# Optimization experiments

Measured on AMD Instinct MI355X. Metric: run time of the kernel, lower is better.

Reference implementation:

```python
import jax, jax.numpy as jnp
import numpy as np

EMBED_DIM = 512
U_EMBED = 6
NUM_HEADS = 8
HEAD_DIM = EMBED_DIM // NUM_HEADS
SCALE = HEAD_DIM ** -0.5
BS, N = 8, 1024


def setup_inputs() -> dict:
    key = jax.random.key(0)
    ks = jax.random.split(key, 9)
    x = jax.random.normal(ks[0], (BS, N, EMBED_DIM), dtype=jnp.float32)
    u = jax.random.normal(ks[1], (BS, U_EMBED, N, N), dtype=jnp.float32)
    umask = jax.random.randint(ks[2], (BS, N, N, 1), 0, 2).astype(bool)
    s = EMBED_DIM ** -0.5
    Wq = jax.random.normal(ks[3], (EMBED_DIM, EMBED_DIM), dtype=jnp.float32) * s
    Wk = jax.random.normal(ks[4], (EMBED_DIM, EMBED_DIM), dtype=jnp.float32) * s
    Wv = jax.random.normal(ks[5], (EMBED_DIM, EMBED_DIM), dtype=jnp.float32) * s
    Wu = jax.random.normal(ks[6], (NUM_HEADS, U_EMBED), dtype=jnp.float32) * (U_EMBED ** -0.5)
    bu = jnp.zeros((NUM_HEADS,), dtype=jnp.float32)
    Wo = jax.random.normal(ks[7], (EMBED_DIM, EMBED_DIM), dtype=jnp.float32) * s
    bo = jnp.zeros((EMBED_DIM,), dtype=jnp.float32)
    return {"x": x, "u": u, "umask": umask, "Wq": Wq, "Wk": Wk, "Wv": Wv,
            "Wu": Wu, "bu": bu, "Wo": Wo, "bo": bo}


def reference(x, u, umask, Wq, Wk, Wv, Wu, bu, Wo, bo):
    bs, n, _ = x.shape
    # projections (torch Linear: y = x @ W.T)
    Q = (x @ Wq.T).reshape(bs, n, NUM_HEADS, HEAD_DIM)
    K = (x @ Wk.T).reshape(bs, n, NUM_HEADS, HEAD_DIM)
    V = (x @ Wv.T).reshape(bs, n, NUM_HEADS, HEAD_DIM)
    # scores: [bs, H, N, N]
    scores = jnp.einsum('bqhd,bkhd->bhqk', Q, K) * SCALE
    # 1x1 conv bias: [bs, u_embed, N, N] -> [bs, H, N, N]
    ub = jnp.einsum('bunm,hu->bhnm', u, Wu) + bu[None, :, None, None]
    # umask: [bs, N, N, 1] -> transpose(3,1) -> [bs, 1, N, N]
    m = jnp.transpose(umask, (0, 3, 2, 1))
    ub = jnp.where(m, -jnp.inf, ub)
    scores = scores + ub
    attn = jax.nn.softmax(scores, axis=-1)
    ctx = jnp.einsum('bhqk,bkhd->bqhd', attn, V).reshape(bs, n, EMBED_DIM)
    out = ctx @ Wo.T + bo
    return out, attn
```

## Files before the change

### kernel.cpp

```cpp
#include <hip/hip_runtime.h>
#include <hip/hip_bf16.h>
#include <math.h>

#define BSZ 8
#define SEQ 1024
#define EMB 512
#define NH 8
#define HD 64
#define UE 6
#define QKSCALE 0.125f

typedef unsigned short u16;
typedef short bf16x8 __attribute__((ext_vector_type(8)));
typedef float f32x4 __attribute__((ext_vector_type(4)));
typedef unsigned short ushort4_t __attribute__((ext_vector_type(4)));

__device__ __forceinline__ u16 f2bf(float f) {
  unsigned u = __float_as_uint(f);
  unsigned r = (u + 0x7fffu + ((u >> 16) & 1u)) >> 16;
  return (u16)r;
}
__device__ __forceinline__ void f2hl(float f, u16& hi, u16& lo) {
  hi = f2bf(f);
  float fh = __uint_as_float(((unsigned)hi) << 16);
  lo = f2bf(f - fh);
}
#define F2HL_V(fv, hv, lv, idx)            \
  {                                        \
    u16 _h, _l;                            \
    f2hl((fv), _h, _l);                    \
    (hv)[idx] = (short)_h;                 \
    (lv)[idx] = (short)_l;                 \
  }
__device__ __forceinline__ f32x4 mfma_bf16(bf16x8 a, bf16x8 b, f32x4 c) {
  return __builtin_amdgcn_mfma_f32_16x16x32_bf16(a, b, c, 0, 0, 0);
}

__global__ __launch_bounds__(256) void split_kernel(const float* __restrict__ src,
                                                    u16* __restrict__ hi, u16* __restrict__ lo, int n4) {
  int i = blockIdx.x * 256 + threadIdx.x;
  if (i >= n4) return;
  float4 v = ((const float4*)src)[i];
  ushort4_t h, l;
  F2HL_V(v.x, h, l, 0); F2HL_V(v.y, h, l, 1);
  F2HL_V(v.z, h, l, 2); F2HL_V(v.w, h, l, 3);
  ((ushort4_t*)hi)[i] = h;
  ((ushort4_t*)lo)[i] = l;
}

__global__ __launch_bounds__(256, 2) void qkv_mfma_kernel(
    const float* __restrict__ x, const u16* __restrict__ Wsp,
    u16* __restrict__ Qhi, u16* __restrict__ Qlo,
    u16* __restrict__ Khi, u16* __restrict__ Klo, u16* __restrict__ Vt) {
  const int mt = blockIdx.x, h = blockIdx.y, wsel = blockIdx.z;
  const int m0 = mt * 64, c0 = h * 64;
  const u16* __restrict__ WH = Wsp + (size_t)wsel * 524288;
  const u16* __restrict__ WL = WH + 262144;
  __shared__ u16 AH[64][40], AL[64][40], BH[64][40], BL[64][40];
  __shared__ u16 vout[64][69];
  const int t = threadIdx.x, w = t >> 6, l = t & 63;
  const int wr = (w >> 1) * 32, wc = (w & 1) * 32;
  f32x4 acc[2][2] = {};
  const int srow = t >> 2;
  for (int e0 = 0; e0 < EMB; e0 += 32) {
    {
      const int c = (t & 3) * 8;
      float4 v0 = *(const float4*)&x[(size_t)(m0 + srow) * EMB + e0 + c];
      float4 v1 = *(const float4*)&x[(size_t)(m0 + srow) * EMB + e0 + c + 4];
      ushort4_t h0, l0, h1, l1;
      F2HL_V(v0.x, h0, l0, 0); F2HL_V(v0.y, h0, l0, 1); F2HL_V(v0.z, h0, l0, 2); F2HL_V(v0.w, h0, l0, 3);
      F2HL_V(v1.x, h1, l1, 0); F2HL_V(v1.y, h1, l1, 1); F2HL_V(v1.z, h1, l1, 2); F2HL_V(v1.w, h1, l1, 3);
      *(ushort4_t*)&AH[srow][c] = h0; *(ushort4_t*)&AH[srow][c + 4] = h1;
      *(ushort4_t*)&AL[srow][c] = l0; *(ushort4_t*)&AL[srow][c + 4] = l1;
      *(bf16x8*)&BH[srow][c] = *(const bf16x8*)&WH[(size_t)(c0 + srow) * EMB + e0 + c];
      *(bf16x8*)&BL[srow][c] = *(const bf16x8*)&WL[(size_t)(c0 + srow) * EMB + e0 + c];
    }
    __syncthreads();
    const int ar = l & 15, ach = (l >> 4) << 3;
    bf16x8 ah0 = *(bf16x8*)&AH[wr + ar][ach],      ah1 = *(bf16x8*)&AH[wr + 16 + ar][ach];
    bf16x8 al0 = *(bf16x8*)&AL[wr + ar][ach],      al1 = *(bf16x8*)&AL[wr + 16 + ar][ach];
    bf16x8 bh0 = *(bf16x8*)&BH[wc + ar][ach],      bh1 = *(bf16x8*)&BH[wc + 16 + ar][ach];
    bf16x8 bl0 = *(bf16x8*)&BL[wc + ar][ach],      bl1 = *(bf16x8*)&BL[wc + 16 + ar][ach];
    acc[0][0] = mfma_bf16(ah0, bh0, acc[0][0]); acc[0][0] = mfma_bf16(ah0, bl0, acc[0][0]); acc[0][0] = mfma_bf16(al0, bh0, acc[0][0]);
    acc[0][1] = mfma_bf16(ah0, bh1, acc[0][1]); acc[0][1] = mfma_bf16(ah0, bl1, acc[0][1]); acc[0][1] = mfma_bf16(al0, bh1, acc[0][1]);
    acc[1][0] = mfma_bf16(ah1, bh0, acc[1][0]); acc[1][0] = mfma_bf16(ah1, bl0, acc[1][0]); acc[1][0] = mfma_bf16(al1, bh0, acc[1][0]);
    acc[1][1] = mfma_bf16(ah1, bh1, acc[1][1]); acc[1][1] = mfma_bf16(ah1, bl1, acc[1][1]); acc[1][1] = mfma_bf16(al1, bh1, acc[1][1]);
    __syncthreads();
  }
  const int bb = m0 >> 10, n0 = m0 & 1023;
  if (wsel < 2) {
    u16* __restrict__ OH = wsel ? Khi : Qhi;
    u16* __restrict__ OL = wsel ? Klo : Qlo;
#pragma unroll
    for (int i = 0; i < 2; ++i)
#pragma unroll
      for (int j = 0; j < 2; ++j) {
        const int col = wc + 16 * j + (l & 15);
#pragma unroll
        for (int r = 0; r < 4; ++r) {
          const int n = n0 + wr + 16 * i + ((l >> 4) << 2) + r;
          size_t o = ((size_t)(bb * NH + h) * SEQ + n) * HD + col;
          u16 hi, lo; f2hl(acc[i][j][r], hi, lo);
          OH[o] = hi; OL[o] = lo;
        }
      }
  } else {
#pragma unroll
    for (int i = 0; i < 2; ++i)
#pragma unroll
      for (int j = 0; j < 2; ++j) {
        const int col = wc + 16 * j + (l & 15);
#pragma unroll
        for (int r = 0; r < 4; ++r)
          vout[wr + 16 * i + ((l >> 4) << 2) + r][col] = f2bf(acc[i][j][r]);
      }
    __syncthreads();
    const int d = t >> 2, nch = (t & 3) * 16;
    bf16x8 o0, o1;
#pragma unroll
    for (int i = 0; i < 8; ++i) o0[i] = (short)vout[nch + i][d];
#pragma unroll
    for (int i = 0; i < 8; ++i) o1[i] = (short)vout[nch + 8 + i][d];
    size_t dst = ((size_t)(bb * NH + h) * HD + d) * SEQ + n0 + nch;
    *(bf16x8*)&Vt[dst] = o0;
    *(bf16x8*)&Vt[dst + 8] = o1;
  }
}

__global__ __launch_bounds__(256, 2) void scores_kernel(
    const u16* __restrict__ Qhi, const u16* __restrict__ Qlo,
    const u16* __restrict__ Khi, const u16* __restrict__ Klo,
    const float* __restrict__ u, const int* __restrict__ umask,
    const float* __restrict__ Wu, const float* __restrict__ bu,
    float* __restrict__ attn, float2* __restrict__ pairs) {
  const int kt = blockIdx.x, qt = blockIdx.y, b = blockIdx.z;
  const int q0 = qt * 64, k0 = kt * 64;
  __shared__ u16 KsH[64][72], KsL[64][72];
  __shared__ unsigned char ms[64][68];
  const int t = threadIdx.x, w = t >> 6, l = t & 63;
  const int qb = 16 * w + ((l >> 4) << 2);
  const int kl = l & 15;

#pragma unroll
  for (int r = 0; r < 16; ++r) {
    int idx = r * 256 + t; int k = idx >> 6, q = idx & 63;
    ms[k][q] = (unsigned char)(umask[((size_t)b * SEQ + k0 + k) * SEQ + q0 + q] != 0);
  }

  unsigned upk[UE][4][2];
  {
    const float* ubase = u + ((size_t)b * UE * SEQ + q0 + qb) * SEQ + k0 + kl;
#pragma unroll
    for (int uu = 0; uu < UE; ++uu)
#pragma unroll
      for (int tt = 0; tt < 4; ++tt)
#pragma unroll
        for (int p = 0; p < 2; ++p) {
          const float* up = ubase + (size_t)uu * SEQ * SEQ + (size_t)(2 * p) * SEQ + 16 * tt;
          float f0 = up[0], f1 = up[SEQ];
          upk[uu][tt][p] = (unsigned)f2bf(f0) | ((unsigned)f2bf(f1) << 16);
        }
  }

  const int krow_s = t >> 2, kc_s = (t & 3) * 16;
  bf16x8 kpre0, kpre1, kpre2, kpre3;
  {
    const u16* kp = Khi + ((size_t)(b * NH) * SEQ + k0 + krow_s) * HD + kc_s;
    const u16* kq = Klo + ((size_t)(b * NH) * SEQ + k0 + krow_s) * HD + kc_s;
    kpre0 = *(const bf16x8*)kp; kpre1 = *(const bf16x8*)(kp + 8);
    kpre2 = *(const bf16x8*)kq; kpre3 = *(const bf16x8*)(kq + 8);
  }

  for (int h = 0; h < NH; ++h) {
    const int bh = b * NH + h;
    __syncthreads();
    *(bf16x8*)&KsH[krow_s][kc_s] = kpre0;
    *(bf16x8*)&KsH[krow_s][kc_s + 8] = kpre1;
    *(bf16x8*)&KsL[krow_s][kc_s] = kpre2;
    *(bf16x8*)&KsL[krow_s][kc_s + 8] = kpre3;
    if (h < NH - 1) {
      const u16* kp = Khi + ((size_t)(bh + 1) * SEQ + k0 + krow_s) * HD + kc_s;
      const u16* kq = Klo + ((size_t)(bh + 1) * SEQ + k0 + krow_s) * HD + kc_s;
      kpre0 = *(const bf16x8*)kp; kpre1 = *(const bf16x8*)(kp + 8);
      kpre2 = *(const bf16x8*)kq; kpre3 = *(const bf16x8*)(kq + 8);
    }
    __syncthreads();

    const u16* qp = Qhi + ((size_t)bh * SEQ + q0 + 16 * w + (l & 15)) * HD + ((l >> 4) << 3);
    const u16* ql = Qlo + ((size_t)bh * SEQ + q0 + 16 * w + (l & 15)) * HD + ((l >> 4) << 3);
    bf16x8 qh0 = *(const bf16x8*)qp, qh1 = *(const bf16x8*)(qp + 32);
    bf16x8 ql0 = *(const bf16x8*)ql, ql1 = *(const bf16x8*)(ql + 32);
    float wu_[UE];
#pragma unroll
    for (int uu = 0; uu < UE; ++uu) wu_[uu] = Wu[h * UE + uu];
    const float bub = bu[h];
    float* abase = attn + ((size_t)bh * SEQ + q0 + qb) * SEQ + k0 + kl;

    float sv[4][4];
#pragma unroll
    for (int tt = 0; tt < 4; ++tt) {
      const int krow = tt * 16 + (l & 15), kch = (l >> 4) << 3;
      bf16x8 kh0 = *(bf16x8*)&KsH[krow][kch], kh1 = *(bf16x8*)&KsH[krow][kch + 32];
      bf16x8 kl0 = *(bf16x8*)&KsL[krow][kch], kl1 = *(bf16x8*)&KsL[krow][kch + 32];
      f32x4 acc = {0.f, 0.f, 0.f, 0.f};
      acc = mfma_bf16(qh0, kh0, acc); acc = mfma_bf16(qh1, kh1, acc);
      acc = mfma_bf16(qh0, kl0, acc); acc = mfma_bf16(qh1, kl1, acc);
      acc = mfma_bf16(ql0, kh0, acc); acc = mfma_bf16(ql1, kh1, acc);
#pragma unroll
      for (int p = 0; p < 2; ++p) {
        float ubx = bub, uby = bub;
#pragma unroll
        for (int uu = 0; uu < UE; ++uu) {
          unsigned pk = upk[uu][tt][p];
          float flo = __uint_as_float(pk << 16);
          float fhi = __uint_as_float(pk & 0xffff0000u);
          ubx = fmaf(wu_[uu], flo, ubx);
          uby = fmaf(wu_[uu], fhi, uby);
        }
        sv[2 * p + 0][tt] = ms[tt * 16 + kl][qb + 2 * p + 0] ? -INFINITY : acc[2 * p + 0] * QKSCALE + ubx;
        sv[2 * p + 1][tt] = ms[tt * 16 + kl][qb + 2 * p + 1] ? -INFINITY : acc[2 * p + 1] * QKSCALE + uby;
      }
    }
#pragma unroll
    for (int r = 0; r < 4; ++r)
#pragma unroll
      for (int tt = 0; tt < 4; ++tt)
        abase[(size_t)r * SEQ + tt * 16] = sv[r][tt];
#pragma unroll
    for (int r = 0; r < 4; ++r) {
      float m = fmaxf(fmaxf(sv[r][0], sv[r][1]), fmaxf(sv[r][2], sv[r][3]));
#pragma unroll
      for (int o = 1; o <= 8; o <<= 1) m = fmaxf(m, __shfl_xor(m, o));
      float s = __expf(sv[r][0] - m) + __expf(sv[r][1] - m) +
                __expf(sv[r][2] - m) + __expf(sv[r][3] - m);
#pragma unroll
      for (int o = 1; o <= 8; o <<= 1) s += __shfl_xor(s, o);
      if (kl == 0)
        pairs[((size_t)bh * SEQ + q0 + qb + r) * 16 + kt] = make_float2(m, s);
    }
  }
}

__global__ __launch_bounds__(256, 2) void pv_softmax_kernel(
    float* __restrict__ attn, const u16* __restrict__ Vt,
    const float2* __restrict__ pairs, u16* __restrict__ ctx) {
  const int qt = blockIdx.x, bh = blockIdx.y;
  const int q0 = qt * 64;
  __shared__ u16 Pl[64][72], Vs[64][72];
  const int t = threadIdx.x, w = t >> 6, l = t & 63;
  const int row = t >> 2, cc = (t & 3) * 16;
  float* arow = attn + ((size_t)bh * SEQ + q0 + row) * SEQ + cc;

  float M = -INFINITY, S = 0.f;
  {
    const float2* pp = pairs + ((size_t)bh * SEQ + q0 + row) * 16 + (t & 3) * 4;
#pragma unroll
    for (int j = 0; j < 4; ++j) {
      float2 c = pp[j];
      float Mn = fmaxf(M, c.x);
      S = S * __expf(M - Mn) + c.y * __expf(c.x - Mn);
      M = Mn;
    }
#pragma unroll
    for (int o = 1; o <= 2; o <<= 1) {
      float Mo = __shfl_xor(M, o), So = __shfl_xor(S, o);
      float Mn = fmaxf(M, Mo);
      S = S * __expf(M - Mn) + So * __expf(Mo - Mn);
      M = Mn;
    }
  }
  const float inv = 1.0f / S;

  const int wr = (w >> 1) * 32, wc = (w & 1) * 32;
  f32x4 acc[2][2] = {};
  float4 va0 = *(const float4*)(arow + 0), va1 = *(const float4*)(arow + 4);
  float4 va2 = *(const float4*)(arow + 8), va3 = *(const float4*)(arow + 12);
  const u16* vrow = Vt + ((size_t)bh * HD + row) * SEQ + cc;
  bf16x8 vb0 = *(const bf16x8*)vrow, vb1 = *(const bf16x8*)(vrow + 8);

  for (int k0 = 0; k0 < SEQ; k0 += 64) {
    bf16x8 p0, p1;
    float4 p;
    p.x = __expf(va0.x - M) * inv; p.y = __expf(va0.y - M) * inv;
    p.z = __expf(va0.z - M) * inv; p.w = __expf(va0.w - M) * inv;
    *(float4*)(arow + k0 + 0) = p;
    p0[0] = (short)f2bf(p.x); p0[1] = (short)f2bf(p.y); p0[2] = (short)f2bf(p.z); p0[3] = (short)f2bf(p.w);
    p.x = __expf(va1.x - M) * inv; p.y = __expf(va1.y - M) * inv;
    p.z = __expf(va1.z - M) * inv; p.w = __expf(va1.w - M) * inv;
    *(float4*)(arow + k0 + 4) = p;
    p0[4] = (short)f2bf(p.x); p0[5] = (short)f2bf(p.y); p0[6] = (short)f2bf(p.z); p0[7] = (short)f2bf(p.w);
    p.x = __expf(va2.x - M) * inv; p.y = __expf(va2.y - M) * inv;
    p.z = __expf(va2.z - M) * inv; p.w = __expf(va2.w - M) * inv;
    *(float4*)(arow + k0 + 8) = p;
    p1[0] = (short)f2bf(p.x); p1[1] = (short)f2bf(p.y); p1[2] = (short)f2bf(p.z); p1[3] = (short)f2bf(p.w);
    p.x = __expf(va3.x - M) * inv; p.y = __expf(va3.y - M) * inv;
    p.z = __expf(va3.z - M) * inv; p.w = __expf(va3.w - M) * inv;
    *(float4*)(arow + k0 + 12) = p;
    p1[4] = (short)f2bf(p.x); p1[5] = (short)f2bf(p.y); p1[6] = (short)f2bf(p.z); p1[7] = (short)f2bf(p.w);

    *(bf16x8*)&Pl[row][cc] = p0;
    *(bf16x8*)&Pl[row][cc + 8] = p1;
    *(bf16x8*)&Vs[row][cc] = vb0;
    *(bf16x8*)&Vs[row][cc + 8] = vb1;

    if (k0 + 64 < SEQ) {
      va0 = *(const float4*)(arow + k0 + 64);
      va1 = *(const float4*)(arow + k0 + 68);
      va2 = *(const float4*)(arow + k0 + 72);
      va3 = *(const float4*)(arow + k0 + 76);
      vb0 = *(const bf16x8*)(vrow + k0 + 64);
      vb1 = *(const bf16x8*)(vrow + k0 + 72);
    }
    __syncthreads();
#pragma unroll
    for (int kb = 0; kb < 2; ++kb) {
      const int kch = kb * 32 + ((l >> 4) << 3);
      bf16x8 a0 = *(bf16x8*)&Pl[wr + (l & 15)][kch];
      bf16x8 a1 = *(bf16x8*)&Pl[wr + 16 + (l & 15)][kch];
      bf16x8 b0 = *(bf16x8*)&Vs[wc + (l & 15)][kch];
      bf16x8 b1 = *(bf16x8*)&Vs[wc + 16 + (l & 15)][kch];
      acc[0][0] = mfma_bf16(a0, b0, acc[0][0]);
      acc[0][1] = mfma_bf16(a0, b1, acc[0][1]);
      acc[1][0] = mfma_bf16(a1, b0, acc[1][0]);
      acc[1][1] = mfma_bf16(a1, b1, acc[1][1]);
    }
    __syncthreads();
  }
  const int b = bh >> 3, h = bh & 7;
#pragma unroll
  for (int i = 0; i < 2; ++i)
#pragma unroll
    for (int j = 0; j < 2; ++j) {
      const int d = h * HD + wc + 16 * j + (l & 15);
#pragma unroll
      for (int r = 0; r < 4; ++r) {
        const int q = q0 + wr + 16 * i + ((l >> 4) << 2) + r;
        ctx[((size_t)(b * SEQ + q)) * EMB + d] = f2bf(acc[i][j][r]);
      }
    }
}

__global__ __launch_bounds__(256, 2) void oproj_kernel(
    const u16* __restrict__ ctx,
    const u16* __restrict__ WoH, const u16* __restrict__ WoL,
    const float* __restrict__ bo, float* __restrict__ out) {
  const int mt = blockIdx.x, ct = blockIdx.y;
  const int m0 = mt * 64, c0 = ct * 64;
  __shared__ u16 AH[64][40], BH[64][40], BL[64][40];
  const int t = threadIdx.x, w = t >> 6, l = t & 63;
  const int wr = (w >> 1) * 32, wc = (w & 1) * 32;
  f32x4 acc[2][2] = {};
  const int srow = t >> 2, sc = (t & 3) * 8;
  for (int e0 = 0; e0 < EMB; e0 += 32) {
    *(bf16x8*)&AH[srow][sc] = *(const bf16x8*)&ctx[(size_t)(m0 + srow) * EMB + e0 + sc];
    *(bf16x8*)&BH[srow][sc] = *(const bf16x8*)&WoH[(size_t)(c0 + srow) * EMB + e0 + sc];
    *(bf16x8*)&BL[srow][sc] = *(const bf16x8*)&WoL[(size_t)(c0 + srow) * EMB + e0 + sc];
    __syncthreads();
    const int ar = l & 15, ach = (l >> 4) << 3;
    bf16x8 ah0 = *(bf16x8*)&AH[wr + ar][ach],      ah1 = *(bf16x8*)&AH[wr + 16 + ar][ach];
    bf16x8 bh0 = *(bf16x8*)&BH[wc + ar][ach],      bh1 = *(bf16x8*)&BH[wc + 16 + ar][ach];
    bf16x8 bl0 = *(bf16x8*)&BL[wc + ar][ach],      bl1 = *(bf16x8*)&BL[wc + 16 + ar][ach];
    acc[0][0] = mfma_bf16(ah0, bh0, acc[0][0]); acc[0][0] = mfma_bf16(ah0, bl0, acc[0][0]);
    acc[0][1] = mfma_bf16(ah0, bh1, acc[0][1]); acc[0][1] = mfma_bf16(ah0, bl1, acc[0][1]);
    acc[1][0] = mfma_bf16(ah1, bh0, acc[1][0]); acc[1][0] = mfma_bf16(ah1, bl0, acc[1][0]);
    acc[1][1] = mfma_bf16(ah1, bh1, acc[1][1]); acc[1][1] = mfma_bf16(ah1, bl1, acc[1][1]);
    __syncthreads();
  }
#pragma unroll
  for (int i = 0; i < 2; ++i)
#pragma unroll
    for (int j = 0; j < 2; ++j) {
      const int col = c0 + wc + 16 * j + (l & 15);
      const float bias = bo[col];
#pragma unroll
      for (int r = 0; r < 4; ++r) {
        const int m = m0 + wr + 16 * i + ((l >> 4) << 2) + r;
        out[(size_t)m * EMB + col] = acc[i][j][r] + bias;
      }
    }
}

extern "C" void kernel_launch(void* const* d_in, const int* in_sizes, int n_in,
                              void* d_out, int out_size, void* d_ws, size_t ws_size,
                              hipStream_t stream) {
  const float* x = (const float*)d_in[0];
  const float* u = (const float*)d_in[1];
  const int* umask = (const int*)d_in[2];
  const float* Wq = (const float*)d_in[3];
  const float* Wk = (const float*)d_in[4];
  const float* Wv = (const float*)d_in[5];
  const float* Wu = (const float*)d_in[6];
  const float* bu = (const float*)d_in[7];
  const float* Wo = (const float*)d_in[8];
  const float* bo = (const float*)d_in[9];

  float* out = (float*)d_out;
  float* attn = out + (size_t)BSZ * SEQ * EMB;

  const size_t per = (size_t)BSZ * NH * SEQ * HD;
  u16* ws = (u16*)d_ws;
  u16* Qhi = ws;
  u16* Qlo = Qhi + per;
  u16* Khi = Qlo + per;
  u16* Klo = Khi + per;
  u16* Vt = Klo + per;
  u16* ctx = Vt + per;
  float2* pairs = (float2*)(ctx + per);
  u16* Wsp = (u16*)((char*)pairs + (size_t)BSZ * NH * SEQ * 16 * sizeof(float2));

  const int wn4 = 262144 / 4;
  split_kernel<<<dim3(wn4 / 256), 256, 0, stream>>>(Wq, Wsp + 0 * 524288, Wsp + 0 * 524288 + 262144, wn4);
  split_kernel<<<dim3(wn4 / 256), 256, 0, stream>>>(Wk, Wsp + 1 * 524288, Wsp + 1 * 524288 + 262144, wn4);
  split_kernel<<<dim3(wn4 / 256), 256, 0, stream>>>(Wv, Wsp + 2 * 524288, Wsp + 2 * 524288 + 262144, wn4);
  split_kernel<<<dim3(wn4 / 256), 256, 0, stream>>>(Wo, Wsp + 3 * 524288, Wsp + 3 * 524288 + 262144, wn4);

  qkv_mfma_kernel<<<dim3(128, 8, 3), 256, 0, stream>>>(x, Wsp, Qhi, Qlo, Khi, Klo, Vt);
  scores_kernel<<<dim3(16, 16, 8), 256, 0, stream>>>(Qhi, Qlo, Khi, Klo, u, umask, Wu, bu, attn, pairs);
  pv_softmax_kernel<<<dim3(16, 64), 256, 0, stream>>>(attn, Vt, pairs, ctx);
  oproj_kernel<<<dim3(128, 8), 256, 0, stream>>>(ctx, Wsp + 3 * 524288, Wsp + 3 * 524288 + 262144, bo, out);
}
```

Before: 421.7 us.

## Store unnormalized bf16 exp scores in-place in attn upper half, drop max tracking

The scores kernel now writes exp(score) directly as bf16 into the upper half of each attn row's float storage and records per-tile plain sums, dropping the running max. The pv kernel reads these bf16 values instead of fp32 scores, writes normalized fp32 attn, and applies 1/sum to the context accumulator at the end. K staging through shared memory is removed in favour of direct global loads, and occupancy hints are raised. The intent is to halve the intermediate score traffic and remove the max bookkeeping, at the cost of possible exp overflow without max subtraction and bf16 precision on the stored attn.

```diff
diff --git a/kernel.cpp b/kernel.cpp
--- a/kernel.cpp
+++ b/kernel.cpp
@@ -19,6 +19,9 @@
   unsigned u = __float_as_uint(f);
   unsigned r = (u + 0x7fffu + ((u >> 16) & 1u)) >> 16;
   return (u16)r;
+}
+__device__ __forceinline__ float bf2f(u16 v) {
+  return __uint_as_float(((unsigned)v) << 16);
 }
 __device__ __forceinline__ void f2hl(float f, u16& hi, u16& lo) {
   hi = f2bf(f);
@@ -127,19 +130,18 @@
   }
 }
 
-__global__ __launch_bounds__(256, 2) void scores_kernel(
+__global__ __launch_bounds__(256, 3) void scores_kernel(
     const u16* __restrict__ Qhi, const u16* __restrict__ Qlo,
     const u16* __restrict__ Khi, const u16* __restrict__ Klo,
     const float* __restrict__ u, const int* __restrict__ umask,
     const float* __restrict__ Wu, const float* __restrict__ bu,
-    float* __restrict__ attn, float2* __restrict__ pairs) {
+    u16* __restrict__ praw, float* __restrict__ sums) {
   const int kt = blockIdx.x, qt = blockIdx.y, b = blockIdx.z;
   const int q0 = qt * 64, k0 = kt * 64;
-  __shared__ u16 KsH[64][72], KsL[64][72];
   __shared__ unsigned char ms[64][68];
   const int t = threadIdx.x, w = t >> 6, l = t & 63;
-  const int qb = 16 * w + ((l >> 4) << 2);
-  const int kl = l & 15;
+  const int kl = l & 15, g = l >> 4;
+  const int qb = 16 * w + (g << 2);
 
 #pragma unroll
   for (int r = 0; r < 16; ++r) {
@@ -148,63 +150,39 @@
   }
 
   unsigned upk[UE][4][2];
-  {
-    const float* ubase = u + ((size_t)b * UE * SEQ + q0 + qb) * SEQ + k0 + kl;
-#pragma unroll
-    for (int uu = 0; uu < UE; ++uu)
-#pragma unroll
-      for (int tt = 0; tt < 4; ++tt)
-#pragma unroll
-        for (int p = 0; p < 2; ++p) {
-          const float* up = ubase + (size_t)uu * SEQ * SEQ + (size_t)(2 * p) * SEQ + 16 * tt;
-          float f0 = up[0], f1 = up[SEQ];
-          upk[uu][tt][p] = (unsigned)f2bf(f0) | ((unsigned)f2bf(f1) << 16);
-        }
-  }
-
-  const int krow_s = t >> 2, kc_s = (t & 3) * 16;
-  bf16x8 kpre0, kpre1, kpre2, kpre3;
-  {
-    const u16* kp = Khi + ((size_t)(b * NH) * SEQ + k0 + krow_s) * HD + kc_s;
-    const u16* kq = Klo + ((size_t)(b * NH) * SEQ + k0 + krow_s) * HD + kc_s;
-    kpre0 = *(const bf16x8*)kp; kpre1 = *(const bf16x8*)(kp + 8);
-    kpre2 = *(const bf16x8*)kq; kpre3 = *(const bf16x8*)(kq + 8);
-  }
+  const float* ubase = u + ((size_t)b * UE * SEQ + q0 + qb) * SEQ + k0 + kl;
+#pragma unroll
+  for (int uu = 0; uu < UE; ++uu)
+#pragma unroll
+    for (int tt = 0; tt < 4; ++tt)
+#pragma unroll
+      for (int p = 0; p < 2; ++p) {
+        const float* up = ubase + (size_t)uu * SEQ * SEQ + (size_t)(2 * p) * SEQ + 16 * tt;
+        upk[uu][tt][p] = (unsigned)f2bf(up[0]) | ((unsigned)f2bf(up[SEQ]) << 16);
+      }
+  __syncthreads();
 
   for (int h = 0; h < NH; ++h) {
     const int bh = b * NH + h;
-    __syncthreads();
-    *(bf16x8*)&KsH[krow_s][kc_s] = kpre0;
-    *(bf16x8*)&KsH[krow_s][kc_s + 8] = kpre1;
-    *(bf16x8*)&KsL[krow_s][kc_s] = kpre2;
-    *(bf16x8*)&KsL[krow_s][kc_s + 8] = kpre3;
-    if (h < NH - 1) {
-      const u16* kp = Khi + ((size_t)(bh + 1) * SEQ + k0 + krow_s) * HD + kc_s;
-      const u16* kq = Klo + ((size_t)(bh + 1) * SEQ + k0 + krow_s) * HD + kc_s;
-      kpre0 = *(const bf16x8*)kp; kpre1 = *(const bf16x8*)(kp + 8);
-      kpre2 = *(const bf16x8*)kq; kpre3 = *(const bf16x8*)(kq + 8);
-    }
-    __syncthreads();
-
-    const u16* qp = Qhi + ((size_t)bh * SEQ + q0 + 16 * w + (l & 15)) * HD + ((l >> 4) << 3);
-    const u16* ql = Qlo + ((size_t)bh * SEQ + q0 + 16 * w + (l & 15)) * HD + ((l >> 4) << 3);
+    const u16* qp = Qhi + ((size_t)bh * SEQ + q0 + 16 * w + kl) * HD + (g << 3);
+    const u16* ql = Qlo + ((size_t)bh * SEQ + q0 + 16 * w + kl) * HD + (g << 3);
     bf16x8 qh0 = *(const bf16x8*)qp, qh1 = *(const bf16x8*)(qp + 32);
     bf16x8 ql0 = *(const bf16x8*)ql, ql1 = *(const bf16x8*)(ql + 32);
     float wu_[UE];
 #pragma unroll
     for (int uu = 0; uu < UE; ++uu) wu_[uu] = Wu[h * UE + uu];
     const float bub = bu[h];
-    float* abase = attn + ((size_t)bh * SEQ + q0 + qb) * SEQ + k0 + kl;
-
-    float sv[4][4];
+    u16* pbase = praw + ((size_t)(bh * SEQ + q0 + qb)) * 2048 + 1024 + k0 + kl;
+    float esum[4] = {0.f, 0.f, 0.f, 0.f};
 #pragma unroll
     for (int tt = 0; tt < 4; ++tt) {
-      const int krow = tt * 16 + (l & 15), kch = (l >> 4) << 3;
-      bf16x8 kh0 = *(bf16x8*)&KsH[krow][kch], kh1 = *(bf16x8*)&KsH[krow][kch + 32];
-      bf16x8 kl0 = *(bf16x8*)&KsL[krow][kch], kl1 = *(bf16x8*)&KsL[krow][kch + 32];
+      const u16* kp = Khi + ((size_t)bh * SEQ + k0 + tt * 16 + kl) * HD + (g << 3);
+      const u16* kq = Klo + ((size_t)bh * SEQ + k0 + tt * 16 + kl) * HD + (g << 3);
+      bf16x8 kh0 = *(const bf16x8*)kp, kh1 = *(const bf16x8*)(kp + 32);
+      bf16x8 kb0 = *(const bf16x8*)kq, kb1 = *(const bf16x8*)(kq + 32);
       f32x4 acc = {0.f, 0.f, 0.f, 0.f};
       acc = mfma_bf16(qh0, kh0, acc); acc = mfma_bf16(qh1, kh1, acc);
-      acc = mfma_bf16(qh0, kl0, acc); acc = mfma_bf16(qh1, kl1, acc);
+      acc = mfma_bf16(qh0, kb0, acc); acc = mfma_bf16(qh1, kb1, acc);
       acc = mfma_bf16(ql0, kh0, acc); acc = mfma_bf16(ql1, kh1, acc);
 #pragma unroll
       for (int p = 0; p < 2; ++p) {
@@ -212,102 +190,84 @@
 #pragma unroll
         for (int uu = 0; uu < UE; ++uu) {
           unsigned pk = upk[uu][tt][p];
-          float flo = __uint_as_float(pk << 16);
-          float fhi = __uint_as_float(pk & 0xffff0000u);
-          ubx = fmaf(wu_[uu], flo, ubx);
-          uby = fmaf(wu_[uu], fhi, uby);
+          ubx = fmaf(wu_[uu], __uint_as_float(pk << 16), ubx);
+          uby = fmaf(wu_[uu], __uint_as_float(pk & 0xffff0000u), uby);
         }
-        sv[2 * p + 0][tt] = ms[tt * 16 + kl][qb + 2 * p + 0] ? -INFINITY : acc[2 * p + 0] * QKSCALE + ubx;
-        sv[2 * p + 1][tt] = ms[tt * 16 + kl][qb + 2 * p + 1] ? -INFINITY : acc[2 * p + 1] * QKSCALE + uby;
+        float v0 = acc[2 * p] * QKSCALE + ubx;
+        float v1 = acc[2 * p + 1] * QKSCALE + uby;
+        u16 e0 = ms[tt * 16 + kl][qb + 2 * p]     ? (u16)0 : f2bf(__expf(v0));
+        u16 e1 = ms[tt * 16 + kl][qb + 2 * p + 1] ? (u16)0 : f2bf(__expf(v1));
+        pbase[(size_t)(2 * p) * 2048 + tt * 16]     = e0;
+        pbase[(size_t)(2 * p + 1) * 2048 + tt * 16] = e1;
+        esum[2 * p]     += bf2f(e0);
+        esum[2 * p + 1] += bf2f(e1);
       }
     }
 #pragma unroll
     for (int r = 0; r < 4; ++r)
 #pragma unroll
-      for (int tt = 0; tt < 4; ++tt)
-        abase[(size_t)r * SEQ + tt * 16] = sv[r][tt];
-#pragma unroll
-    for (int r = 0; r < 4; ++r) {
-      float m = fmaxf(fmaxf(sv[r][0], sv[r][1]), fmaxf(sv[r][2], sv[r][3]));
-#pragma unroll
-      for (int o = 1; o <= 8; o <<= 1) m = fmaxf(m, __shfl_xor(m, o));
-      float s = __expf(sv[r][0] - m) + __expf(sv[r][1] - m) +
-                __expf(sv[r][2] - m) + __expf(sv[r][3] - m);
-#pragma unroll
-      for (int o = 1; o <= 8; o <<= 1) s += __shfl_xor(s, o);
-      if (kl == 0)
-        pairs[((size_t)bh * SEQ + q0 + qb + r) * 16 + kt] = make_float2(m, s);
-    }
-  }
-}
-
-__global__ __launch_bounds__(256, 2) void pv_softmax_kernel(
-    float* __restrict__ attn, const u16* __restrict__ Vt,
-    const float2* __restrict__ pairs, u16* __restrict__ ctx) {
+      for (int o = 1; o <= 8; o <<= 1) esum[r] += __shfl_xor(esum[r], o);
+    if (kl == 0) {
+#pragma unroll
+      for (int r = 0; r < 4; ++r)
+        sums[((size_t)bh * SEQ + q0 + qb + r) * 16 + kt] = esum[r];
+    }
+  }
+}
+
+__global__ __launch_bounds__(256, 4) void pv_softmax_kernel(
+    float* attn, const u16* __restrict__ Vt,
+    const float* __restrict__ sums, u16* __restrict__ ctx) {
   const int qt = blockIdx.x, bh = blockIdx.y;
   const int q0 = qt * 64;
   __shared__ u16 Pl[64][72], Vs[64][72];
+  __shared__ float invl[64];
   const int t = threadIdx.x, w = t >> 6, l = t & 63;
   const int row = t >> 2, cc = (t & 3) * 16;
-  float* arow = attn + ((size_t)bh * SEQ + q0 + row) * SEQ + cc;
-
-  float M = -INFINITY, S = 0.f;
+
+  float S = 0.f;
   {
-    const float2* pp = pairs + ((size_t)bh * SEQ + q0 + row) * 16 + (t & 3) * 4;
-#pragma unroll
-    for (int j = 0; j < 4; ++j) {
-      float2 c = pp[j];
-      float Mn = fmaxf(M, c.x);
-      S = S * __expf(M - Mn) + c.y * __expf(c.x - Mn);
-      M = Mn;
-    }
-#pragma unroll
-    for (int o = 1; o <= 2; o <<= 1) {
-      float Mo = __shfl_xor(M, o), So = __shfl_xor(S, o);
-      float Mn = fmaxf(M, Mo);
-      S = S * __expf(M - Mn) + So * __expf(Mo - Mn);
-      M = Mn;
-    }
+    const float* sp = sums + ((size_t)bh * SEQ + q0 + row) * 16 + (t & 3) * 4;
+#pragma unroll
+    for (int j = 0; j < 4; ++j) S += sp[j];
+#pragma unroll
+    for (int o = 1; o <= 2; o <<= 1) S += __shfl_xor(S, o);
   }
   const float inv = 1.0f / S;
+  if ((t & 3) == 0) invl[row] = inv;
+
+  const u16* prow = (const u16*)attn + ((size_t)(bh * SEQ + q0 + row)) * 2048 + 1024;
+  float* arow = attn + ((size_t)(bh * SEQ + q0 + row)) * SEQ;
+  const u16* vrow = Vt + ((size_t)bh * HD + row) * SEQ + cc;
 
   const int wr = (w >> 1) * 32, wc = (w & 1) * 32;
   f32x4 acc[2][2] = {};
-  float4 va0 = *(const float4*)(arow + 0), va1 = *(const float4*)(arow + 4);
-  float4 va2 = *(const float4*)(arow + 8), va3 = *(const float4*)(arow + 12);
-  const u16* vrow = Vt + ((size_t)bh * HD + row) * SEQ + cc;
+  bf16x8 pa = *(const bf16x8*)&prow[cc], pb = *(const bf16x8*)&prow[cc + 8];
   bf16x8 vb0 = *(const bf16x8*)vrow, vb1 = *(const bf16x8*)(vrow + 8);
 
   for (int k0 = 0; k0 < SEQ; k0 += 64) {
-    bf16x8 p0, p1;
-    float4 p;
-    p.x = __expf(va0.x - M) * inv; p.y = __expf(va0.y - M) * inv;
-    p.z = __expf(va0.z - M) * inv; p.w = __expf(va0.w - M) * inv;
-    *(float4*)(arow + k0 + 0) = p;
-    p0[0] = (short)f2bf(p.x); p0[1] = (short)f2bf(p.y); p0[2] = (short)f2bf(p.z); p0[3] = (short)f2bf(p.w);
-    p.x = __expf(va1.x - M) * inv; p.y = __expf(va1.y - M) * inv;
-    p.z = __expf(va1.z - M) * inv; p.w = __expf(va1.w - M) * inv;
-    *(float4*)(arow + k0 + 4) = p;
-    p0[4] = (short)f2bf(p.x); p0[5] = (short)f2bf(p.y); p0[6] = (short)f2bf(p.z); p0[7] = (short)f2bf(p.w);
-    p.x = __expf(va2.x - M) * inv; p.y = __expf(va2.y - M) * inv;
-    p.z = __expf(va2.z - M) * inv; p.w = __expf(va2.w - M) * inv;
-    *(float4*)(arow + k0 + 8) = p;
-    p1[0] = (short)f2bf(p.x); p1[1] = (short)f2bf(p.y); p1[2] = (short)f2bf(p.z); p1[3] = (short)f2bf(p.w);
-    p.x = __expf(va3.x - M) * inv; p.y = __expf(va3.y - M) * inv;
-    p.z = __expf(va3.z - M) * inv; p.w = __expf(va3.w - M) * inv;
-    *(float4*)(arow + k0 + 12) = p;
-    p1[4] = (short)f2bf(p.x); p1[5] = (short)f2bf(p.y); p1[6] = (short)f2bf(p.z); p1[7] = (short)f2bf(p.w);
-
-    *(bf16x8*)&Pl[row][cc] = p0;
-    *(bf16x8*)&Pl[row][cc + 8] = p1;
+    float* ap = arow + k0 + cc;
+    {
+      float4 o0, o1, o2, o3;
+      o0.x = bf2f((u16)pa[0]) * inv; o0.y = bf2f((u16)pa[1]) * inv;
+      o0.z = bf2f((u16)pa[2]) * inv; o0.w = bf2f((u16)pa[3]) * inv;
+      o1.x = bf2f((u16)pa[4]) * inv; o1.y = bf2f((u16)pa[5]) * inv;
+      o1.z = bf2f((u16)pa[6]) * inv; o1.w = bf2f((u16)pa[7]) * inv;
+      o2.x = bf2f((u16)pb[0]) * inv; o2.y = bf2f((u16)pb[1]) * inv;
+      o2.z = bf2f((u16)pb[2]) * inv; o2.w = bf2f((u16)pb[3]) * inv;
+      o3.x = bf2f((u16)pb[4]) * inv; o3.y = bf2f((u16)pb[5]) * inv;
+      o3.z = bf2f((u16)pb[6]) * inv; o3.w = bf2f((u16)pb[7]) * inv;
+      ((float4*)ap)[0] = o0; ((float4*)ap)[1] = o1;
+      ((float4*)ap)[2] = o2; ((float4*)ap)[3] = o3;
+    }
+    *(bf16x8*)&Pl[row][cc] = pa;
+    *(bf16x8*)&Pl[row][cc + 8] = pb;
     *(bf16x8*)&Vs[row][cc] = vb0;
     *(bf16x8*)&Vs[row][cc + 8] = vb1;
 
     if (k0 + 64 < SEQ) {
-      va0 = *(const float4*)(arow + k0 + 64);
-      va1 = *(const float4*)(arow + k0 + 68);
-      va2 = *(const float4*)(arow + k0 + 72);
-      va3 = *(const float4*)(arow + k0 + 76);
+      pa = *(const bf16x8*)&prow[k0 + 64 + cc];
+      pb = *(const bf16x8*)&prow[k0 + 64 + cc + 8];
       vb0 = *(const bf16x8*)(vrow + k0 + 64);
       vb1 = *(const bf16x8*)(vrow + k0 + 72);
     }
@@ -334,8 +294,8 @@
       const int d = h * HD + wc + 16 * j + (l & 15);
 #pragma unroll
       for (int r = 0; r < 4; ++r) {
-        const int q = q0 + wr + 16 * i + ((l >> 4) << 2) + r;
-        ctx[((size_t)(b * SEQ + q)) * EMB + d] = f2bf(acc[i][j][r]);
+        const int ql_ = wr + 16 * i + ((l >> 4) << 2) + r;
+        ctx[((size_t)(b * SEQ + q0 + ql_)) * EMB + d] = f2bf(acc[i][j][r] * invl[ql_]);
       }
     }
 }
@@ -405,8 +365,8 @@
   u16* Klo = Khi + per;
   u16* Vt = Klo + per;
   u16* ctx = Vt + per;
-  float2* pairs = (float2*)(ctx + per);
-  u16* Wsp = (u16*)((char*)pairs + (size_t)BSZ * NH * SEQ * 16 * sizeof(float2));
+  float* sums = (float*)(ctx + per);
+  u16* Wsp = (u16*)(sums + (size_t)BSZ * NH * SEQ * 16);
 
   const int wn4 = 262144 / 4;
   split_kernel<<<dim3(wn4 / 256), 256, 0, stream>>>(Wq, Wsp + 0 * 524288, Wsp + 0 * 524288 + 262144, wn4);
@@ -415,7 +375,8 @@
   split_kernel<<<dim3(wn4 / 256), 256, 0, stream>>>(Wo, Wsp + 3 * 524288, Wsp + 3 * 524288 + 262144, wn4);
 
   qkv_mfma_kernel<<<dim3(128, 8, 3), 256, 0, stream>>>(x, Wsp, Qhi, Qlo, Khi, Klo, Vt);
-  scores_kernel<<<dim3(16, 16, 8), 256, 0, stream>>>(Qhi, Qlo, Khi, Klo, u, umask, Wu, bu, attn, pairs);
-  pv_softmax_kernel<<<dim3(16, 64), 256, 0, stream>>>(attn, Vt, pairs, ctx);
+  scores_kernel<<<dim3(16, 16, 8), 256, 0, stream>>>(Qhi, Qlo, Khi, Klo, u, umask, Wu, bu,
+                                                     (u16*)attn, sums);
+  pv_softmax_kernel<<<dim3(16, 64), 256, 0, stream>>>(attn, Vt, sums, ctx);
   oproj_kernel<<<dim3(128, 8), 256, 0, stream>>>(ctx, Wsp + 3 * 524288, Wsp + 3 * 524288 + 262144, bo, out);
 }
```

Result: slower. 452.6 us (+7.3%).
